# Kernel tuning notes

Measured on AMD Instinct MI355X. Metric: run time of the kernel, lower is better.

## Reference

```python
import jax, jax.numpy as jnp
import numpy as np

B, H, N, D = 64, 12, 196, 768  # ViT-B/16 @ 224: 196 patch tokens + 1 CLS


def setup_inputs() -> dict:
    key = jax.random.key(0)
    k1, k2, k3 = jax.random.split(key, 3)
    student_tokens = jax.random.normal(k1, (B, N, D), dtype=jnp.float32)
    teacher_tokens = jax.random.normal(k2, (B, N, D), dtype=jnp.float32)
    teacher_attn = jax.random.uniform(k3, (B, H, N + 1, N + 1), dtype=jnp.float32)
    return {
        "student_tokens": student_tokens,
        "teacher_tokens": teacher_tokens,
        "teacher_attn": teacher_attn,
    }


def reference(student_tokens, teacher_tokens, teacher_attn):
    s = student_tokens.astype(jnp.float32)
    t = teacher_tokens.astype(jnp.float32)
    # CLS->patch attention, averaged over heads: [B, N]
    w = teacher_attn[:, :, 0, 1:].mean(axis=1)
    w = w / (w.sum(axis=-1, keepdims=True) + 1e-8)
    s = w[..., None] * s
    t = w[..., None] * t
    # center over token dim
    s_c = s - s.mean(axis=1, keepdims=True)
    t_c = t - t.mean(axis=1, keepdims=True)
    tr_s = jnp.sum(s_c * s_c, axis=(1, 2))  # [B]
    tr_t = jnp.sum(t_c * t_c, axis=(1, 2))  # [B]
    # cross-covariance: [B, D, D]
    cross = jnp.einsum("bnd,bne->bde", s_c, t_c)
    # nuclear norm = sum of singular values
    nuclear = jnp.linalg.svd(cross, compute_uv=False).sum(axis=-1)  # [B]
    loss = jnp.maximum(tr_s + tr_t - 2.0 * nuclear, 0.0).mean()
    return loss
```

## Files before the change

### kernel.cpp

```cpp
#include <hip/hip_runtime.h>
#include <hip/hip_bf16.h>
#include <math.h>

#define NTOK 196
#define NDIM 768
#define NB 64
#define NH 12
#define NA 197
#define MAT (NTOK * NTOK)
#define ATTN_HW (NA * NA)
#define POLAR_ITERS 15

#define PADC 208
#define NTILE 13
#define POLAR_LDS_BYTES (2 * NTOK * PADC * 2)

#define GCH 64
#define GPLANE (208 * GCH)
#define GRAM_LDS_BYTES (2 * GPLANE * 2)

#define POW_LD 197
#define POW_F_WORDS (NTOK * POW_LD)
#define POW_LDS_BYTES ((POW_F_WORDS + 2 * NTOK + 256) * 4)

#define PTLD 208
#define TRI_WORDS 19306
#define CHOL2_PT_WORDS (16 * PTLD)
#define CHOL2_TRI_OFF CHOL2_PT_WORDS
#define CHOL2_ROWOFF_OFF (CHOL2_TRI_OFF + TRI_WORDS)
#define CHOL2_PV_OFF 22832
#define CHOL2_LDS_BYTES ((CHOL2_PV_OFF + 32) * 4)

typedef __attribute__((ext_vector_type(8))) short short8;
typedef __attribute__((ext_vector_type(4))) short short4_t;
typedef __attribute__((ext_vector_type(4))) float f32x4;

__device__ inline short8 s8zero() { short8 z = {0,0,0,0,0,0,0,0}; return z; }

__device__ inline short f2bf(float f) {
  union { float f; unsigned u; } v; v.f = f;
  unsigned u = v.u;
  u += 0x7fffu + ((u >> 16) & 1u);
  return (short)(u >> 16);
}
__device__ inline float bf2f(short s) {
  union { unsigned u; float f; } v;
  v.u = ((unsigned)(unsigned short)s) << 16;
  return v.f;
}

__global__ void k_w(const float* __restrict__ attn, float* __restrict__ wbuf) {
  int b = blockIdx.x;
  int tid = threadIdx.x;
  __shared__ float red[256];
  float w0 = 0.f;
  if (tid < NTOK) {
    size_t base = (size_t)b * NH * ATTN_HW + 1 + tid;
    #pragma unroll
    for (int h = 0; h < NH; ++h) w0 += attn[base + (size_t)h * ATTN_HW];
    w0 *= (1.f / NH);
  }
  red[tid] = (tid < NTOK) ? w0 : 0.f;
  __syncthreads();
  for (int s = 128; s > 0; s >>= 1) { if (tid < s) red[tid] += red[tid + s]; __syncthreads(); }
  float S = red[0];
  if (tid < NTOK) wbuf[b * NTOK + tid] = w0 / (S + 1e-8f);
}

__global__ __launch_bounds__(512, 1) void k_gram_mfma(
    const float* __restrict__ s, const float* __restrict__ t,
    const float* __restrict__ wbuf, float* __restrict__ Gbuf) {
  extern __shared__ short gsm[];
  short* bhp = gsm;
  short* blp = gsm + GPLANE;
  __shared__ float wsh[NTOK];
  int slot = blockIdx.x, b = slot >> 1, src = slot & 1;
  const float* X = (src ? t : s) + (size_t)b * NTOK * NDIM;
  int tid = threadIdx.x;
  int wave = tid >> 6, ln15 = tid & 15, quad = (tid >> 4) & 3;

  if (tid < NTOK) wsh[tid] = wbuf[b * NTOK + tid];
  for (int i = tid; i < 768; i += 512) {
    int p = i / 384, o = i - p * 384;
    ((int*)(gsm + p * GPLANE + 196 * GCH))[o] = 0;
  }
  __syncthreads();

  f32x4 zz = {0.f, 0.f, 0.f, 0.f};
  f32x4 acc[12];
  #pragma unroll
  for (int j = 0; j < 12; ++j) acc[j] = zz;

  for (int c = 0; c < NDIM / GCH; ++c) {
    int kc = c * GCH;
    for (int gi = tid; gi < NTOK * 8; gi += 512) {
      int r = gi >> 3, g = gi & 7;
      const float* sp = X + (size_t)r * NDIM + kc + g * 8;
      float4 f0 = *(const float4*)(sp);
      float4 f1 = *(const float4*)(sp + 4);
      float wv = wsh[r];
      float vs[8] = {f0.x, f0.y, f0.z, f0.w, f1.x, f1.y, f1.z, f1.w};
      short8 hv, lv;
      #pragma unroll
      for (int e = 0; e < 8; ++e) {
        float y = wv * vs[e];
        short hb = f2bf(y);
        hv[e] = hb;
        lv[e] = f2bf(y - bf2f(hb));
      }
      int pg = (g ^ (r & 7)) * 8;
      *(short8*)(bhp + r * GCH + pg) = hv;
      *(short8*)(blp + r * GCH + pg) = lv;
    }
    __syncthreads();
    #pragma unroll
    for (int j = 0; j < 12; ++j) {
      int T = wave + 8 * j;
      if (T < 91) {
        int ti = (int)((sqrtf(8.f * T + 1.f) - 1.f) * 0.5f);
        if ((ti + 1) * (ti + 2) / 2 <= T) ++ti;
        if (ti * (ti + 1) / 2 > T) --ti;
        int tj = T - ti * (ti + 1) / 2;
        int ra = ti * 16 + ln15, rb = tj * 16 + ln15;
        #pragma unroll
        for (int ks = 0; ks < 2; ++ks) {
          int gb0 = ks * 4 + quad;
          int ga = (gb0 ^ (ra & 7)) * 8, gb = (gb0 ^ (rb & 7)) * 8;
          short8 ah = *(const short8*)(bhp + ra * GCH + ga);
          short8 al = *(const short8*)(blp + ra * GCH + ga);
          short8 bhf = *(const short8*)(bhp + rb * GCH + gb);
          short8 blf = *(const short8*)(blp + rb * GCH + gb);
          acc[j] = __builtin_amdgcn_mfma_f32_16x16x32_bf16(ah, bhf, acc[j], 0, 0, 0);
          acc[j] = __builtin_amdgcn_mfma_f32_16x16x32_bf16(ah, blf, acc[j], 0, 0, 0);
          acc[j] = __builtin_amdgcn_mfma_f32_16x16x32_bf16(al, bhf, acc[j], 0, 0, 0);
        }
      }
    }
    __syncthreads();
  }

  float* G = Gbuf + (size_t)slot * MAT;
  #pragma unroll
  for (int j = 0; j < 12; ++j) {
    int T = wave + 8 * j;
    if (T < 91) {
      int ti = (int)((sqrtf(8.f * T + 1.f) - 1.f) * 0.5f);
      if ((ti + 1) * (ti + 2) / 2 <= T) ++ti;
      if (ti * (ti + 1) / 2 > T) --ti;
      int tj = T - ti * (ti + 1) / 2;
      int col = tj * 16 + ln15;
      #pragma unroll
      for (int r = 0; r < 4; ++r) {
        int row = ti * 16 + quad * 4 + r;
        if (row < NTOK && col < NTOK) {
          G[row * NTOK + col] = acc[j][r];
          if (ti != tj) G[col * NTOK + row] = acc[j][r];
        }
      }
    }
  }
}

__global__ void k_center(float* __restrict__ Gbuf, float* __restrict__ trPb) {
  int slot = blockIdx.x;
  float* A = Gbuf + (size_t)slot * MAT;
  __shared__ float r[NTOK];
  __shared__ float red[256];
  __shared__ float gsh, dsh;
  int tid = threadIdx.x;
  float acc = 0.f;
  if (tid < NTOK) {
    for (int m = 0; m < NTOK; ++m) acc += A[m * NTOK + tid];
    r[tid] = acc * (1.f / NTOK);
  }
  red[tid] = (tid < NTOK) ? acc * (1.f / NTOK) : 0.f;
  __syncthreads();
  for (int s = 128; s > 0; s >>= 1) { if (tid < s) red[tid] += red[tid + s]; __syncthreads(); }
  float g = red[0] * (1.f / NTOK);
  float tv = (tid < NTOK) ? (A[tid * NTOK + tid] - 2.f * r[tid] + g) : 0.f;
  __syncthreads();
  red[tid] = tv;
  __syncthreads();
  for (int s = 128; s > 0; s >>= 1) { if (tid < s) red[tid] += red[tid + s]; __syncthreads(); }
  if (tid == 0) {
    float tr = red[0];
    trPb[slot] = tr;
    gsh = g;
    dsh = 1e-4f * fmaxf(tr, 0.f) * (1.f / NTOK);
  }
  __syncthreads();
  float gg = gsh, dd = dsh;
  for (int idx = tid; idx < MAT; idx += 256) {
    int n = idx / NTOK, m = idx - n * NTOK;
    float v = A[idx] - r[n] - r[m] + gg;
    if (n == m) v += dd;
    A[idx] = v;
  }
}

__global__ __launch_bounds__(256, 1) void k_chol_panel(float* __restrict__ Gbuf) {
  extern __shared__ float smf[];
  float* Pt = smf;
  float* tri = smf + CHOL2_TRI_OFF;
  int* rowoff = (int*)(smf + CHOL2_ROWOFF_OFF);
  float* pvb = smf + CHOL2_PV_OFF;
  int slot = blockIdx.x;
  float* A = Gbuf + (size_t)slot * MAT;
  int tid = threadIdx.x;
  if (tid < NTOK) rowoff[tid] = tid * (tid + 1) / 2;
  __syncthreads();
  for (int idx = tid; idx < MAT; idx += 256) {
    int i = idx / NTOK, j = idx - i * NTOK;
    if (j <= i) tri[rowoff[i] + j] = A[idx];
  }
  __syncthreads();

  for (int k0 = 0; k0 < NTOK; k0 += 16) {
    int nb = (NTOK - k0 < 16) ? (NTOK - k0) : 16;
    int t = tid;
    int i = k0 + t;
    bool hasrow = (t < NTOK - k0);
    int ro = hasrow ? rowoff[i] : 0;

    float a[16];
    #pragma unroll
    for (int jj = 0; jj < 16; ++jj) a[jj] = 0.f;
    if (hasrow) {
      #pragma unroll
      for (int jj = 0; jj < 16; ++jj)
        if (jj < nb && k0 + jj <= i) a[jj] = tri[ro + k0 + jj];
    }

    #pragma unroll
    for (int jj = 0; jj < 16; ++jj) {
      bool cv = (jj < nb);
      if (cv && hasrow && t >= jj && t < nb) pvb[((jj & 1) << 4) + t] = a[jj];
      __syncthreads();
      if (cv && hasrow && t >= jj) {
        const float* pv = pvb + ((jj & 1) << 4);
        f32x4 p0 = *(const f32x4*)(pv);
        f32x4 p1 = *(const f32x4*)(pv + 4);
        f32x4 p2 = *(const f32x4*)(pv + 8);
        f32x4 p3 = *(const f32x4*)(pv + 12);
        float pvj = (jj < 4) ? p0[jj & 3] : (jj < 8) ? p1[jj & 3]
                   : (jj < 12) ? p2[jj & 3] : p3[jj & 3];
        float sq = sqrtf(fmaxf(pvj, 1e-20f));
        float pivinv = 1.f / sq;
        float v = a[jj] * pivinv;
        a[jj] = v;
        #pragma unroll
        for (int m = 0; m < 16; ++m) {
          if (m > jj) {
            float pvm = (m < 4) ? p0[m & 3] : (m < 8) ? p1[m & 3]
                       : (m < 12) ? p2[m & 3] : p3[m & 3];
            if (m < nb) a[m] -= v * (pvm * pivinv);
          }
        }
      }
    }

    if (hasrow) {
      #pragma unroll
      for (int jj = 0; jj < 16; ++jj)
        if (jj < nb && k0 + jj <= i) tri[ro + k0 + jj] = a[jj];
      if (t >= nb) {
        #pragma unroll
        for (int jj = 0; jj < 16; ++jj)
          if (jj < nb) Pt[jj * PTLD + i] = a[jj];
      }
    }
    __syncthreads();

    int k1 = k0 + nb;
    int nrem = NTOK - k1;
    if (nrem > 0) {
      int ntile = (nrem + 3) >> 2;
      int Ttot = ntile * (ntile + 1) / 2;
      for (int T = tid; T < Ttot; T += 256) {
        float disc = (2.f * ntile + 1.f) * (2.f * ntile + 1.f) - 8.f * (float)T;
        int tm = (int)((2.f * ntile + 1.f - sqrtf(fmaxf(disc, 0.f))) * 0.5f);
        if (tm > ntile - 1) tm = ntile - 1;
        if (tm < 0) tm = 0;
        #define FCOL(c) ((c) * ntile - (((c) * ((c) - 1)) >> 1))
        while (tm + 1 <= ntile - 1 && FCOL(tm + 1) <= T) ++tm;
        while (tm > 0 && FCOL(tm) > T) --tm;
        int ti = tm + (T - FCOL(tm));
        #undef FCOL
        int i0 = k1 + ti * 4, m0 = k1 + tm * 4;
        f32x4 acc0 = {0.f, 0.f, 0.f, 0.f};
        f32x4 acc1 = acc0, acc2 = acc0, acc3 = acc0;
        #pragma unroll
        for (int jj = 0; jj < 16; ++jj) {
          if (jj < nb) {
            f32x4 li = *(const f32x4*)(Pt + jj * PTLD + i0);
            f32x4 lm = *(const f32x4*)(Pt + jj * PTLD + m0);
            acc0 += lm * li[0];
            acc1 += lm * li[1];
            acc2 += lm * li[2];
            acc3 += lm * li[3];
          }
        }
        #define STORE_ROW(r, av)                                        \
          { int ii = i0 + (r);                                          \
            if (ii < NTOK) {                                            \
              int roi = rowoff[ii];                                     \
              if (m0 + 0 <= ii) tri[roi + m0 + 0] -= (av)[0];           \
              if (m0 + 1 <= ii) tri[roi + m0 + 1] -= (av)[1];           \
              if (m0 + 2 <= ii) tri[roi + m0 + 2] -= (av)[2];           \
              if (m0 + 3 <= ii) tri[roi + m0 + 3] -= (av)[3];           \
            } }
        STORE_ROW(0, acc0)
        STORE_ROW(1, acc1)
        STORE_ROW(2, acc2)
        STORE_ROW(3, acc3)
        #undef STORE_ROW
      }
    }
    __syncthreads();
  }

  for (int idx = tid; idx < MAT; idx += 256) {
    int i = idx / NTOK, j = idx - i * NTOK;
    A[idx] = (j <= i) ? tri[rowoff[i] + j] : 0.f;
  }
}

__global__ void k_chol_global(float* __restrict__ Gbuf) {
  int slot = blockIdx.x;
  float* A = Gbuf + (size_t)slot * MAT;
  __shared__ float col[NTOK];
  __shared__ float piv;
  int tid = threadIdx.x;
  for (int k = 0; k < NTOK; ++k) {
    if (tid == 0) { float p = sqrtf(fmaxf(A[k * NTOK + k], 1e-20f)); A[k * NTOK + k] = p; piv = p; }
    __syncthreads();
    float inv = 1.f / piv;
    for (int i = k + 1 + tid; i < NTOK; i += 256) {
      float v = A[i * NTOK + k] * inv;
      A[i * NTOK + k] = v;
      col[i] = v;
    }
    for (int j = k + 1 + tid; j < NTOK; j += 256) A[k * NTOK + j] = 0.f;
    __syncthreads();
    int nrem = NTOK - 1 - k;
    int total = nrem * (nrem + 1) / 2;
    for (int tt = tid; tt < total; tt += 256) {
      int a = (int)((sqrtf(8.f * tt + 1.f) - 1.f) * 0.5f);
      while ((a + 1) * (a + 2) / 2 <= tt) ++a;
      while (a * (a + 1) / 2 > tt) --a;
      int bb = tt - a * (a + 1) / 2;
      int i = k + 1 + a, j = k + 1 + bb;
      A[i * NTOK + j] -= col[i] * col[j];
    }
    __syncthreads();
  }
}

__global__ void k_F(const float* __restrict__ Gbuf, float* __restrict__ Fbuf) {
  int b = blockIdx.y;
  const float* Lp = Gbuf + (size_t)(2 * b) * MAT;
  const float* Lq = Gbuf + (size_t)(2 * b + 1) * MAT;
  int ti = blockIdx.x / 7, tj = blockIdx.x % 7;
  int ri = ti * 32, cj = tj * 32;
  __shared__ float As[32][33], Bs[32][33];
  int tid = threadIdx.x, ty = tid >> 4, tx = tid & 15;
  float a00 = 0, a01 = 0, a10 = 0, a11 = 0;
  for (int k0 = 0; k0 < NTOK; k0 += 32) {
    for (int l = tid; l < 1024; l += 256) {
      int kk = l >> 5, ii = l & 31;
      int krow = k0 + kk;
      As[kk][ii] = (krow < NTOK && ri + ii < NTOK) ? Lp[(size_t)krow * NTOK + ri + ii] : 0.f;
      Bs[kk][ii] = (krow < NTOK && cj + ii < NTOK) ? Lq[(size_t)krow * NTOK + cj + ii] : 0.f;
    }
    __syncthreads();
    #pragma unroll
    for (int kk = 0; kk < 32; ++kk) {
      float p0 = As[kk][ty], p1 = As[kk][ty + 16];
      float q0 = Bs[kk][tx], q1 = Bs[kk][tx + 16];
      a00 += p0 * q0; a01 += p0 * q1; a10 += p1 * q0; a11 += p1 * q1;
    }
    __syncthreads();
  }
  float* F = Fbuf + (size_t)b * MAT;
  int i0 = ri + ty, i1 = ri + ty + 16, j0 = cj + tx, j1 = cj + tx + 16;
  if (i0 < NTOK && j0 < NTOK) F[i0 * NTOK + j0] = a00;
  if (i0 < NTOK && j1 < NTOK) F[i0 * NTOK + j1] = a01;
  if (i1 < NTOK && j0 < NTOK) F[i1 * NTOK + j0] = a10;
  if (i1 < NTOK && j1 < NTOK) F[i1 * NTOK + j1] = a11;
}

__global__ __launch_bounds__(256, 1) void k_pow_lds(const float* __restrict__ Fbuf,
                                                    float* __restrict__ nrmb) {
  extern __shared__ float psm[];
  float* Fsh = psm;
  float* v = psm + POW_F_WORDS;
  float* u = v + NTOK;
  float* red = u + NTOK;
  int b = blockIdx.x;
  const float* F = Fbuf + (size_t)b * MAT;
  int tid = threadIdx.x;
  for (int idx = tid; idx < MAT; idx += 256) {
    int i = idx / NTOK, j = idx - i * NTOK;
    Fsh[i * POW_LD + j] = F[idx];
  }
  if (tid < NTOK) v[tid] = 1.f;
  __syncthreads();
  float lastsum = 1.f;
  for (int it = 0; it < 6; ++it) {
    if (tid < NTOK) {
      float a = 0.f;
      for (int j = 0; j < NTOK; ++j) a += Fsh[tid * POW_LD + j] * v[j];
      u[tid] = a;
    }
    __syncthreads();
    float a2 = 0.f;
    if (tid < NTOK) { for (int i = 0; i < NTOK; ++i) a2 += Fsh[i * POW_LD + tid] * u[i]; }
    red[tid] = (tid < NTOK) ? a2 * a2 : 0.f;
    __syncthreads();
    for (int s2 = 128; s2 > 0; s2 >>= 1) { if (tid < s2) red[tid] += red[tid + s2]; __syncthreads(); }
    float sum = red[0];
    lastsum = sum;
    float invn = rsqrtf(sum + 1e-30f);
    __syncthreads();
    if (tid < NTOK) v[tid] = a2 * invn;
    __syncthreads();
  }
  if (tid == 0) {
    float sig = sqrtf(sqrtf(lastsum));
    nrmb[b] = 1.f / (1.1f * sig + 1e-30f);
  }
}

__global__ void k_pow(const float* __restrict__ Fbuf, float* __restrict__ nrmb) {
  int b = blockIdx.x;
  const float* F = Fbuf + (size_t)b * MAT;
  __shared__ float v[NTOK], u[NTOK];
  __shared__ float red[256];
  int tid = threadIdx.x;
  if (tid < NTOK) v[tid] = 1.f;
  __syncthreads();
  float lastsum = 1.f;
  for (int it = 0; it < 6; ++it) {
    float a = 0.f;
    if (tid < NTOK) { for (int j = 0; j < NTOK; ++j) a += F[tid * NTOK + j] * v[j]; }
    __syncthreads();
    if (tid < NTOK) u[tid] = a;
    __syncthreads();
    float a2 = 0.f;
    if (tid < NTOK) { for (int i = 0; i < NTOK; ++i) a2 += F[i * NTOK + tid] * u[i]; }
    red[tid] = (tid < NTOK) ? a2 * a2 : 0.f;
    __syncthreads();
    for (int s = 128; s > 0; s >>= 1) { if (tid < s) red[tid] += red[tid + s]; __syncthreads(); }
    float sum = red[0];
    lastsum = sum;
    float invn = rsqrtf(sum + 1e-30f);
    __syncthreads();
    if (tid < NTOK) v[tid] = a2 * invn;
    __syncthreads();
  }
  if (tid == 0) {
    float sig = sqrtf(sqrtf(lastsum));
    nrmb[b] = 1.f / (1.1f * sig + 1e-30f);
  }
}

__global__ void k_scale(const float* __restrict__ Fbuf, const float* __restrict__ nrmb,
                        float* __restrict__ X) {
  int b = blockIdx.y;
  int idx = blockIdx.x * 256 + threadIdx.x;
  if (idx < MAT) X[(size_t)b * MAT + idx] = Fbuf[(size_t)b * MAT + idx] * nrmb[b];
}

__global__ __launch_bounds__(512, 1) void k_polar_fused(
    const float* __restrict__ Fbuf, const float* __restrict__ nrmb,
    float* __restrict__ Xout) {
  extern __shared__ short sm[];
  short* bufA = sm;
  short* bufB = sm + NTOK * PADC;
  int b = blockIdx.x;
  const float* F = Fbuf + (size_t)b * MAT;
  float* XO = Xout + (size_t)b * MAT;
  int tid = threadIdx.x;
  int wave = tid >> 6, ln15 = tid & 15, quad = (tid >> 4) & 3;
  int rt0 = wave, rt1 = wave + 8;
  bool has2 = (rt1 < NTILE);

  for (int q = tid; q < (2 * NTOK * PADC) / 8; q += 512) {
    int4 z = {0, 0, 0, 0};
    ((int4*)sm)[q] = z;
  }
  __syncthreads();
  float invc = nrmb[b];
  for (int q = tid; q < MAT / 4; q += 512) {
    int idx = q * 4;
    int i = idx / NTOK, j = idx - i * NTOK;
    float4 f = ((const float4*)F)[q];
    short4_t w;
    w[0] = f2bf(f.x * invc); w[1] = f2bf(f.y * invc);
    w[2] = f2bf(f.z * invc); w[3] = f2bf(f.w * invc);
    *(short4_t*)(bufA + i * PADC + j) = w;
  }
  __syncthreads();

  int arow0 = rt0 * 16 + ln15;
  int arow1 = rt1 * 16 + ln15;
  bool av1 = has2 && (arow1 < NTOK);
  int m0a = rt0 * 16 + quad * 4;
  int m1a = rt1 * 16 + quad * 4;

  for (int it = 0; it < POLAR_ITERS; ++it) {
    short8 g0[7], g1[7];
    #pragma unroll
    for (int ks = 0; ks < 7; ++ks) {
      int kk = ks * 32 + quad * 8;
      short8 v0 = s8zero(), v1 = s8zero();
      if (kk < PADC) {
        #pragma unroll
        for (int j = 0; j < 8; ++j) {
          v0[j] = bufA[(kk + j) * PADC + arow0];
          if (has2) v1[j] = bufA[(kk + j) * PADC + arow1];
        }
      }
      g0[ks] = v0; g1[ks] = v1;
    }
    {
      short8 a0[7], a1[7];
      #pragma unroll
      for (int ks = 0; ks < 7; ++ks) {
        int kk = ks * 32 + quad * 8;
        a0[ks] = (kk < PADC) ? *(const short8*)(bufA + arow0 * PADC + kk) : s8zero();
        a1[ks] = (av1 && kk < PADC) ? *(const short8*)(bufA + arow1 * PADC + kk) : s8zero();
      }
      for (int ct = 0; ct < NTILE; ++ct) {
        int brow = ct * 16 + ln15;
        bool bv = brow < NTOK;
        f32x4 acc0 = {0.f, 0.f, 0.f, 0.f};
        f32x4 acc1 = {0.f, 0.f, 0.f, 0.f};
        if (ct == rt0) {
          #pragma unroll
          for (int ks = 0; ks < 7; ++ks) {
            acc0 = __builtin_amdgcn_mfma_f32_16x16x32_bf16(a0[ks], a0[ks], acc0, 0, 0, 0);
            if (has2)
              acc1 = __builtin_amdgcn_mfma_f32_16x16x32_bf16(a1[ks], a0[ks], acc1, 0, 0, 0);
          }
        } else if (has2 && ct == rt1) {
          #pragma unroll
          for (int ks = 0; ks < 7; ++ks) {
            acc0 = __builtin_amdgcn_mfma_f32_16x16x32_bf16(a0[ks], a1[ks], acc0, 0, 0, 0);
            acc1 = __builtin_amdgcn_mfma_f32_16x16x32_bf16(a1[ks], a1[ks], acc1, 0, 0, 0);
          }
        } else {
          #pragma unroll
          for (int ks = 0; ks < 7; ++ks) {
            int kk = ks * 32 + quad * 8;
            short8 bfr = (bv && kk < PADC) ? *(const short8*)(bufA + brow * PADC + kk)
                                           : s8zero();
            acc0 = __builtin_amdgcn_mfma_f32_16x16x32_bf16(a0[ks], bfr, acc0, 0, 0, 0);
            if (has2)
              acc1 = __builtin_amdgcn_mfma_f32_16x16x32_bf16(a1[ks], bfr, acc1, 0, 0, 0);
          }
        }
        if (bv) {
          short4_t w0;
          #pragma unroll
          for (int r = 0; r < 4; ++r) {
            float h = -0.5f * acc0[r] + ((m0a + r == brow) ? 1.5f : 0.f);
            w0[r] = f2bf(h);
          }
          *(short4_t*)(bufB + brow * PADC + m0a) = w0;
          if (has2) {
            short4_t w1;
            #pragma unroll
            for (int r = 0; r < 4; ++r) {
              float h = -0.5f * acc1[r] + ((m1a + r == brow) ? 1.5f : 0.f);
              w1[r] = f2bf(h);
            }
            *(short4_t*)(bufB + brow * PADC + m1a) = w1;
          }
        }
      }
    }
    __syncthreads();
    {
      for (int ct = 0; ct < NTILE; ++ct) {
        int n = ct * 16 + ln15;
        bool nv = n < NTOK;
        f32x4 acc0 = {0.f, 0.f, 0.f, 0.f};
        f32x4 acc1 = {0.f, 0.f, 0.f, 0.f};
        #pragma unroll
        for (int ks = 0; ks < 7; ++ks) {
          int kk = ks * 32 + quad * 8;
          short8 bfr = (nv && kk < PADC) ? *(const short8*)(bufB + n * PADC + kk)
                                         : s8zero();
          acc0 = __builtin_amdgcn_mfma_f32_16x16x32_bf16(g0[ks], bfr, acc0, 0, 0, 0);
          if (has2)
            acc1 = __builtin_amdgcn_mfma_f32_16x16x32_bf16(g1[ks], bfr, acc1, 0, 0, 0);
        }
        if (nv) {
          short4_t w0;
          #pragma unroll
          for (int r = 0; r < 4; ++r) w0[r] = f2bf(acc0[r]);
          *(short4_t*)(bufA + n * PADC + m0a) = w0;
          if (has2) {
            short4_t w1;
            #pragma unroll
            for (int r = 0; r < 4; ++r) w1[r] = f2bf(acc1[r]);
            *(short4_t*)(bufA + n * PADC + m1a) = w1;
          }
        }
      }
    }
    __syncthreads();
  }

  for (int q = tid; q < MAT / 4; q += 512) {
    int idx = q * 4;
    int i = idx / NTOK, j = idx - i * NTOK;
    short4_t w = *(const short4_t*)(bufA + i * PADC + j);
    float4 f;
    f.x = bf2f(w[0]); f.y = bf2f(w[1]); f.z = bf2f(w[2]); f.w = bf2f(w[3]);
    ((float4*)XO)[q] = f;
  }
}

__global__ void k_xtx(const float* __restrict__ Xb, float* __restrict__ Gp) {
  int b = blockIdx.y;
  const float* X = Xb + (size_t)b * MAT;
  int x = blockIdx.x, ti = 0;
  while (x >= ti + 1) { x -= ti + 1; ++ti; }
  int tj = x;
  int ri = ti * 32, cj = tj * 32;
  __shared__ float As[32][33], Bs[32][33];
  int tid = threadIdx.x, ty = tid >> 4, tx = tid & 15;
  float a00 = 0, a01 = 0, a10 = 0, a11 = 0;
  for (int k0 = 0; k0 < NTOK; k0 += 32) {
    for (int l = tid; l < 1024; l += 256) {
      int kk = l >> 5, ii = l & 31;
      int krow = k0 + kk;
      As[kk][ii] = (krow < NTOK && ri + ii < NTOK) ? X[(size_t)krow * NTOK + ri + ii] : 0.f;
      Bs[kk][ii] = (krow < NTOK && cj + ii < NTOK) ? X[(size_t)krow * NTOK + cj + ii] : 0.f;
    }
    __syncthreads();
    #pragma unroll
    for (int kk = 0; kk < 32; ++kk) {
      float p0 = As[kk][ty], p1 = As[kk][ty + 16];
      float q0 = Bs[kk][tx], q1 = Bs[kk][tx + 16];
      a00 += p0 * q0; a01 += p0 * q1; a10 += p1 * q0; a11 += p1 * q1;
    }
    __syncthreads();
  }
  float* G = Gp + (size_t)b * MAT;
  int i0 = ri + ty, i1 = ri + ty + 16, j0 = cj + tx, j1 = cj + tx + 16;
  if (i0 < NTOK && j0 < NTOK) { G[i0 * NTOK + j0] = a00; G[j0 * NTOK + i0] = a00; }
  if (i0 < NTOK && j1 < NTOK) { G[i0 * NTOK + j1] = a01; G[j1 * NTOK + i0] = a01; }
  if (i1 < NTOK && j0 < NTOK) { G[i1 * NTOK + j0] = a10; G[j0 * NTOK + i1] = a10; }
  if (i1 < NTOK && j1 < NTOK) { G[i1 * NTOK + j1] = a11; G[j1 * NTOK + i1] = a11; }
}

__global__ void k_nsup(const float* __restrict__ Xb, const float* __restrict__ Gp,
                       float* __restrict__ Xn) {
  int b = blockIdx.y;
  const float* X = Xb + (size_t)b * MAT;
  const float* G = Gp + (size_t)b * MAT;
  int ti = blockIdx.x / 7, tj = blockIdx.x % 7;
  int ri = ti * 32, cj = tj * 32;
  __shared__ float As[32][33], Bs[32][33];
  int tid = threadIdx.x, ty = tid >> 4, tx = tid & 15;
  float a00 = 0, a01 = 0, a10 = 0, a11 = 0;
  for (int k0 = 0; k0 < NTOK; k0 += 32) {
    for (int l = tid; l < 1024; l += 256) {
      int rr = l >> 5, cc = l & 31;
      As[rr][cc] = (ri + rr < NTOK && k0 + cc < NTOK) ? X[(size_t)(ri + rr) * NTOK + k0 + cc] : 0.f;
      Bs[rr][cc] = (k0 + rr < NTOK && cj + cc < NTOK) ? G[(size_t)(k0 + rr) * NTOK + cj + cc] : 0.f;
    }
    __syncthreads();
    #pragma unroll
    for (int kk = 0; kk < 32; ++kk) {
      float p0 = As[ty][kk], p1 = As[ty + 16][kk];
      float q0 = Bs[kk][tx], q1 = Bs[kk][tx + 16];
      a00 += p0 * q0; a01 += p0 * q1; a10 += p1 * q0; a11 += p1 * q1;
    }
    __syncthreads();
  }
  float* O = Xn + (size_t)b * MAT;
  int i0 = ri + ty, i1 = ri + ty + 16, j0 = cj + tx, j1 = cj + tx + 16;
  if (i0 < NTOK && j0 < NTOK) O[i0 * NTOK + j0] = 1.5f * X[i0 * NTOK + j0] - 0.5f * a00;
  if (i0 < NTOK && j1 < NTOK) O[i0 * NTOK + j1] = 1.5f * X[i0 * NTOK + j1] - 0.5f * a01;
  if (i1 < NTOK && j0 < NTOK) O[i1 * NTOK + j0] = 1.5f * X[i1 * NTOK + j0] - 0.5f * a10;
  if (i1 < NTOK && j1 < NTOK) O[i1 * NTOK + j1] = 1.5f * X[i1 * NTOK + j1] - 0.5f * a11;
}

__global__ void k_nuc(const float* __restrict__ U, const float* __restrict__ Fbuf,
                      float* __restrict__ nucb) {
  int b = blockIdx.x;
  int tid = threadIdx.x;
  const float* Ub = U + (size_t)b * MAT;
  const float* Fb = Fbuf + (size_t)b * MAT;
  float acc = 0.f;
  for (int idx = tid; idx < MAT; idx += 256) acc += Ub[idx] * Fb[idx];
  __shared__ float red[256];
  red[tid] = acc;
  __syncthreads();
  for (int s = 128; s > 0; s >>= 1) { if (tid < s) red[tid] += red[tid + s]; __syncthreads(); }
  if (tid == 0) nucb[b] = red[0];
}

__global__ void k_final(const float* __restrict__ trPb, const float* __restrict__ nucb,
                        float* __restrict__ out) {
  int tid = threadIdx.x;
  float v = fmaxf(trPb[2 * tid] + trPb[2 * tid + 1] - 2.f * nucb[tid], 0.f);
  #pragma unroll
  for (int off = 32; off; off >>= 1) v += __shfl_down(v, off);
  if (tid == 0) out[0] = v * (1.f / 64.f);
}

extern "C" void kernel_launch(void* const* d_in, const int* in_sizes, int n_in,
                              void* d_out, int out_size, void* d_ws, size_t ws_size,
                              hipStream_t stream) {
  (void)in_sizes; (void)n_in; (void)out_size; (void)ws_size;
  const float* s = (const float*)d_in[0];
  const float* t = (const float*)d_in[1];
  const float* attn = (const float*)d_in[2];
  float* out = (float*)d_out;

  float* W = (float*)d_ws;
  float* Gbuf = W;
  float* Fbuf = Gbuf + (size_t)128 * MAT;
  float* Xbuf = Fbuf + (size_t)64 * MAT;
  float* Xnew = Xbuf + (size_t)64 * MAT;
  float* Gpol = Xnew + (size_t)64 * MAT;
  float* wbuf = Gpol + (size_t)64 * MAT;
  float* trPb = wbuf + (size_t)NB * NTOK;
  float* nucb = trPb + 128;
  float* nrmb = nucb + 64;

  k_w<<<NB, 256, 0, stream>>>(attn, wbuf);
  k_gram_mfma<<<128, 512, GRAM_LDS_BYTES, stream>>>(s, t, wbuf, Gbuf);
  k_center<<<128, 256, 0, stream>>>(Gbuf, trPb);

  hipError_t chol_ok = hipFuncSetAttribute(
      reinterpret_cast<const void*>(k_chol_panel),
      hipFuncAttributeMaxDynamicSharedMemorySize, CHOL2_LDS_BYTES);
  if (chol_ok == hipSuccess) {
    k_chol_panel<<<128, 256, CHOL2_LDS_BYTES, stream>>>(Gbuf);
  } else {
    k_chol_global<<<128, 256, 0, stream>>>(Gbuf);
  }

  k_F<<<dim3(49, 64), 256, 0, stream>>>(Gbuf, Fbuf);

  hipError_t pow_ok = hipFuncSetAttribute(
      reinterpret_cast<const void*>(k_pow_lds),
      hipFuncAttributeMaxDynamicSharedMemorySize, POW_LDS_BYTES);
  if (pow_ok == hipSuccess) {
    k_pow_lds<<<64, 256, POW_LDS_BYTES, stream>>>(Fbuf, nrmb);
  } else {
    k_pow<<<64, 256, 0, stream>>>(Fbuf, nrmb);
  }

  hipError_t fused_ok = hipFuncSetAttribute(
      reinterpret_cast<const void*>(k_polar_fused),
      hipFuncAttributeMaxDynamicSharedMemorySize, POLAR_LDS_BYTES);

  const float* finalX;
  if (fused_ok == hipSuccess) {
    k_polar_fused<<<NB, 512, POLAR_LDS_BYTES, stream>>>(Fbuf, nrmb, Xbuf);
    k_xtx<<<dim3(28, 64), 256, 0, stream>>>(Xbuf, Gpol);
    k_nsup<<<dim3(49, 64), 256, 0, stream>>>(Xbuf, Gpol, Xnew);
    k_xtx<<<dim3(28, 64), 256, 0, stream>>>(Xnew, Gpol);
    k_nsup<<<dim3(49, 64), 256, 0, stream>>>(Xnew, Gpol, Xbuf);
    finalX = Xbuf;
  } else {
    k_scale<<<dim3(151, 64), 256, 0, stream>>>(Fbuf, nrmb, Xbuf);
    float* Xc = Xbuf;
    float* Xn = Xnew;
    for (int it = 0; it < POLAR_ITERS; ++it) {
      k_xtx<<<dim3(28, 64), 256, 0, stream>>>(Xc, Gpol);
      k_nsup<<<dim3(49, 64), 256, 0, stream>>>(Xc, Gpol, Xn);
      float* tmp = Xc; Xc = Xn; Xn = tmp;
    }
    finalX = Xc;
  }

  k_nuc<<<64, 256, 0, stream>>>(finalX, Fbuf, nucb);
  k_final<<<1, 64, 0, stream>>>(trPb, nucb, out);
}
```

Before: 1.065 ms.

## Compute F = Lp^T Lq with split-bf16 MFMA and transposed Cholesky output

Adds an MFMA kernel for the F product that splits fp32 Cholesky factors into high and low bf16 parts and keeps three cross products, to approximate fp32 accuracy while using matrix cores. The Cholesky kernel can now write its factor transposed so the new kernel reads contiguous rows. The launch uses 2 blocks per batch, which leaves most of the GPU idle. The polar kernel is also reworked: diagonal-tile register reuse is removed, the transposed gather moves after the first barrier with an added sync, and the vectorized float4 and short4 loads and stores become scalar, which may cost bandwidth.

```diff
diff --git a/kernel.cpp b/kernel.cpp
--- a/kernel.cpp
+++ b/kernel.cpp
@@ -18,6 +18,13 @@
 #define GCH 64
 #define GPLANE (208 * GCH)
 #define GRAM_LDS_BYTES (2 * GPLANE * 2)
+
+#define FCH 64
+#define FA_ROWS 208
+#define FB_ROWS 112
+#define FAPLANE (FA_ROWS * FCH)
+#define FBPLANE (FB_ROWS * FCH)
+#define FMF_LDS_BYTES ((2 * FAPLANE + 2 * FBPLANE) * 2)
 
 #define POW_LD 197
 #define POW_F_WORDS (NTOK * POW_LD)
@@ -198,7 +205,8 @@
   }
 }
 
-__global__ __launch_bounds__(256, 1) void k_chol_panel(float* __restrict__ Gbuf) {
+__global__ __launch_bounds__(256, 1) void k_chol_panel(float* __restrict__ Gbuf,
+                                                       int transposeOut) {
   extern __shared__ float smf[];
   float* Pt = smf;
   float* tri = smf + CHOL2_TRI_OFF;
@@ -319,9 +327,16 @@
     __syncthreads();
   }
 
-  for (int idx = tid; idx < MAT; idx += 256) {
-    int i = idx / NTOK, j = idx - i * NTOK;
-    A[idx] = (j <= i) ? tri[rowoff[i] + j] : 0.f;
+  if (transposeOut) {
+    for (int idx = tid; idx < MAT; idx += 256) {
+      int r2 = idx / NTOK, c2 = idx - r2 * NTOK;
+      A[idx] = (r2 <= c2) ? tri[rowoff[c2] + r2] : 0.f;
+    }
+  } else {
+    for (int idx = tid; idx < MAT; idx += 256) {
+      int i = idx / NTOK, j = idx - i * NTOK;
+      A[idx] = (j <= i) ? tri[rowoff[i] + j] : 0.f;
+    }
   }
 }
 
@@ -353,6 +368,113 @@
       A[i * NTOK + j] -= col[i] * col[j];
     }
     __syncthreads();
+  }
+}
+
+__global__ __launch_bounds__(512, 1) void k_F_mfma(const float* __restrict__ Gbuf,
+                                                   float* __restrict__ Fbuf) {
+  extern __shared__ short fsm[];
+  short* Ah = fsm;
+  short* Al = Ah + FAPLANE;
+  short* Bh = Al + FAPLANE;
+  short* Bl = Bh + FBPLANE;
+  int half = blockIdx.x, b = blockIdx.y;
+  const float* LTp = Gbuf + (size_t)(2 * b) * MAT;
+  const float* LTq = Gbuf + (size_t)(2 * b + 1) * MAT;
+  int co = half * 112;
+  int tid = threadIdx.x;
+  int wave = tid >> 6, ln15 = tid & 15, quad = (tid >> 4) & 3;
+
+  f32x4 zz = {0.f, 0.f, 0.f, 0.f};
+  f32x4 acc[12];
+  #pragma unroll
+  for (int j = 0; j < 12; ++j) acc[j] = zz;
+
+  for (int c = 0; c < 4; ++c) {
+    int kc = c * FCH;
+    bool fullchunk = (kc + FCH <= NTOK);
+    for (int gi = tid; gi < (FA_ROWS + FB_ROWS) * 8; gi += 512) {
+      bool isA = gi < FA_ROWS * 8;
+      int li = isA ? gi : gi - FA_ROWS * 8;
+      int r = li >> 3, g = li & 7;
+      int grow = isA ? r : co + r;
+      short8 hv = s8zero(), lv = s8zero();
+      if (grow < NTOK) {
+        const float* src = (isA ? LTp : LTq) + (size_t)grow * NTOK + kc + g * 8;
+        if (fullchunk) {
+          float4 f0 = *(const float4*)(src);
+          float4 f1 = *(const float4*)(src + 4);
+          float vs[8] = {f0.x, f0.y, f0.z, f0.w, f1.x, f1.y, f1.z, f1.w};
+          #pragma unroll
+          for (int e = 0; e < 8; ++e) {
+            short hb = f2bf(vs[e]);
+            hv[e] = hb;
+            lv[e] = f2bf(vs[e] - bf2f(hb));
+          }
+        } else {
+          #pragma unroll
+          for (int e = 0; e < 8; ++e) {
+            int k = kc + g * 8 + e;
+            if (k < NTOK) {
+              float y = src[e];
+              short hb = f2bf(y);
+              hv[e] = hb;
+              lv[e] = f2bf(y - bf2f(hb));
+            }
+          }
+        }
+      }
+      int pg = (g ^ (r & 7)) * 8;
+      if (isA) {
+        *(short8*)(Ah + r * FCH + pg) = hv;
+        *(short8*)(Al + r * FCH + pg) = lv;
+      } else {
+        *(short8*)(Bh + r * FCH + pg) = hv;
+        *(short8*)(Bl + r * FCH + pg) = lv;
+      }
+    }
+    __syncthreads();
+    #pragma unroll
+    for (int j = 0; j < 12; ++j) {
+      int T = wave + 8 * j;
+      if (T < 91) {
+        int ti = T / 7, tj = T - ti * 7;
+        if (co + tj * 16 < NTOK) {
+          int ra = ti * 16 + ln15;
+          int rb = tj * 16 + ln15;
+          #pragma unroll
+          for (int ks = 0; ks < 2; ++ks) {
+            int gb0 = ks * 4 + quad;
+            int ga = (gb0 ^ (ra & 7)) * 8, gb = (gb0 ^ (rb & 7)) * 8;
+            short8 ah = *(const short8*)(Ah + ra * FCH + ga);
+            short8 al = *(const short8*)(Al + ra * FCH + ga);
+            short8 bh = *(const short8*)(Bh + rb * FCH + gb);
+            short8 bl = *(const short8*)(Bl + rb * FCH + gb);
+            acc[j] = __builtin_amdgcn_mfma_f32_16x16x32_bf16(ah, bh, acc[j], 0, 0, 0);
+            acc[j] = __builtin_amdgcn_mfma_f32_16x16x32_bf16(ah, bl, acc[j], 0, 0, 0);
+            acc[j] = __builtin_amdgcn_mfma_f32_16x16x32_bf16(al, bh, acc[j], 0, 0, 0);
+          }
+        }
+      }
+    }
+    __syncthreads();
+  }
+
+  float* F = Fbuf + (size_t)b * MAT;
+  #pragma unroll
+  for (int j = 0; j < 12; ++j) {
+    int T = wave + 8 * j;
+    if (T < 91) {
+      int ti = T / 7, tj = T - ti * 7;
+      int col = co + tj * 16 + ln15;
+      if (col < NTOK) {
+        #pragma unroll
+        for (int r = 0; r < 4; ++r) {
+          int row = ti * 16 + quad * 4 + r;
+          if (row < NTOK) F[row * NTOK + col] = acc[j][r];
+        }
+      }
+    }
   }
 }
 
@@ -485,20 +607,12 @@
   int rt0 = wave, rt1 = wave + 8;
   bool has2 = (rt1 < NTILE);
 
-  for (int q = tid; q < (2 * NTOK * PADC) / 8; q += 512) {
-    int4 z = {0, 0, 0, 0};
-    ((int4*)sm)[q] = z;
-  }
+  for (int i = tid; i < (2 * NTOK * PADC) / 2; i += 512) ((int*)sm)[i] = 0;
   __syncthreads();
   float invc = nrmb[b];
-  for (int q = tid; q < MAT / 4; q += 512) {
-    int idx = q * 4;
+  for (int idx = tid; idx < MAT; idx += 512) {
     int i = idx / NTOK, j = idx - i * NTOK;
-    float4 f = ((const float4*)F)[q];
-    short4_t w;
-    w[0] = f2bf(f.x * invc); w[1] = f2bf(f.y * invc);
-    w[2] = f2bf(f.z * invc); w[3] = f2bf(f.w * invc);
-    *(short4_t*)(bufA + i * PADC + j) = w;
+    bufA[i * PADC + j] = f2bf(F[idx] * invc);
   }
   __syncthreads();
 
@@ -509,20 +623,6 @@
   int m1a = rt1 * 16 + quad * 4;
 
   for (int it = 0; it < POLAR_ITERS; ++it) {
-    short8 g0[7], g1[7];
-    #pragma unroll
-    for (int ks = 0; ks < 7; ++ks) {
-      int kk = ks * 32 + quad * 8;
-      short8 v0 = s8zero(), v1 = s8zero();
-      if (kk < PADC) {
-        #pragma unroll
-        for (int j = 0; j < 8; ++j) {
-          v0[j] = bufA[(kk + j) * PADC + arow0];
-          if (has2) v1[j] = bufA[(kk + j) * PADC + arow1];
-        }
-      }
-      g0[ks] = v0; g1[ks] = v1;
-    }
     {
       short8 a0[7], a1[7];
       #pragma unroll
@@ -536,29 +636,13 @@
         bool bv = brow < NTOK;
         f32x4 acc0 = {0.f, 0.f, 0.f, 0.f};
         f32x4 acc1 = {0.f, 0.f, 0.f, 0.f};
-        if (ct == rt0) {
-          #pragma unroll
-          for (int ks = 0; ks < 7; ++ks) {
-            acc0 = __builtin_amdgcn_mfma_f32_16x16x32_bf16(a0[ks], a0[ks], acc0, 0, 0, 0);
-            if (has2)
-              acc1 = __builtin_amdgcn_mfma_f32_16x16x32_bf16(a1[ks], a0[ks], acc1, 0, 0, 0);
-          }
-        } else if (has2 && ct == rt1) {
-          #pragma unroll
-          for (int ks = 0; ks < 7; ++ks) {
-            acc0 = __builtin_amdgcn_mfma_f32_16x16x32_bf16(a0[ks], a1[ks], acc0, 0, 0, 0);
-            acc1 = __builtin_amdgcn_mfma_f32_16x16x32_bf16(a1[ks], a1[ks], acc1, 0, 0, 0);
-          }
-        } else {
-          #pragma unroll
-          for (int ks = 0; ks < 7; ++ks) {
-            int kk = ks * 32 + quad * 8;
-            short8 bfr = (bv && kk < PADC) ? *(const short8*)(bufA + brow * PADC + kk)
-                                           : s8zero();
-            acc0 = __builtin_amdgcn_mfma_f32_16x16x32_bf16(a0[ks], bfr, acc0, 0, 0, 0);
-            if (has2)
-              acc1 = __builtin_amdgcn_mfma_f32_16x16x32_bf16(a1[ks], bfr, acc1, 0, 0, 0);
-          }
+        #pragma unroll
+        for (int ks = 0; ks < 7; ++ks) {
+          int kk = ks * 32 + quad * 8;
+          short8 bfr = (bv && kk < PADC) ? *(const short8*)(bufA + brow * PADC + kk) : s8zero();
+          acc0 = __builtin_amdgcn_mfma_f32_16x16x32_bf16(a0[ks], bfr, acc0, 0, 0, 0);
+          if (has2)
+            acc1 = __builtin_amdgcn_mfma_f32_16x16x32_bf16(a1[ks], bfr, acc1, 0, 0, 0);
         }
         if (bv) {
           short4_t w0;
@@ -582,6 +666,21 @@
     }
     __syncthreads();
     {
+      short8 g0[7], g1[7];
+      #pragma unroll
+      for (int ks = 0; ks < 7; ++ks) {
+        int kk = ks * 32 + quad * 8;
+        short8 v0 = s8zero(), v1 = s8zero();
+        if (kk < PADC) {
+          #pragma unroll
+          for (int j = 0; j < 8; ++j) {
+            v0[j] = bufA[(kk + j) * PADC + arow0];
+            if (has2) v1[j] = bufA[(kk + j) * PADC + arow1];
+          }
+        }
+        g0[ks] = v0; g1[ks] = v1;
+      }
+      __syncthreads();
       for (int ct = 0; ct < NTILE; ++ct) {
         int n = ct * 16 + ln15;
         bool nv = n < NTOK;
@@ -590,8 +689,7 @@
         #pragma unroll
         for (int ks = 0; ks < 7; ++ks) {
           int kk = ks * 32 + quad * 8;
-          short8 bfr = (nv && kk < PADC) ? *(const short8*)(bufB + n * PADC + kk)
-                                         : s8zero();
+          short8 bfr = (nv && kk < PADC) ? *(const short8*)(bufB + n * PADC + kk) : s8zero();
           acc0 = __builtin_amdgcn_mfma_f32_16x16x32_bf16(g0[ks], bfr, acc0, 0, 0, 0);
           if (has2)
             acc1 = __builtin_amdgcn_mfma_f32_16x16x32_bf16(g1[ks], bfr, acc1, 0, 0, 0);
@@ -613,13 +711,9 @@
     __syncthreads();
   }
 
-  for (int q = tid; q < MAT / 4; q += 512) {
-    int idx = q * 4;
+  for (int idx = tid; idx < MAT; idx += 512) {
     int i = idx / NTOK, j = idx - i * NTOK;
-    short4_t w = *(const short4_t*)(bufA + i * PADC + j);
-    float4 f;
-    f.x = bf2f(w[0]); f.y = bf2f(w[1]); f.z = bf2f(w[2]); f.w = bf2f(w[3]);
-    ((float4*)XO)[q] = f;
+    XO[idx] = bf2f(bufA[i * PADC + j]);
   }
 }
 
@@ -741,13 +835,22 @@
   hipError_t chol_ok = hipFuncSetAttribute(
       reinterpret_cast<const void*>(k_chol_panel),
       hipFuncAttributeMaxDynamicSharedMemorySize, CHOL2_LDS_BYTES);
+  hipError_t fmf_ok = hipFuncSetAttribute(
+      reinterpret_cast<const void*>(k_F_mfma),
+      hipFuncAttributeMaxDynamicSharedMemorySize, FMF_LDS_BYTES);
+  bool mfmaF = (chol_ok == hipSuccess) && (fmf_ok == hipSuccess);
+
   if (chol_ok == hipSuccess) {
-    k_chol_panel<<<128, 256, CHOL2_LDS_BYTES, stream>>>(Gbuf);
+    k_chol_panel<<<128, 256, CHOL2_LDS_BYTES, stream>>>(Gbuf, mfmaF ? 1 : 0);
   } else {
     k_chol_global<<<128, 256, 0, stream>>>(Gbuf);
   }
 
-  k_F<<<dim3(49, 64), 256, 0, stream>>>(Gbuf, Fbuf);
+  if (mfmaF) {
+    k_F_mfma<<<dim3(2, 64), 512, FMF_LDS_BYTES, stream>>>(Gbuf, Fbuf);
+  } else {
+    k_F<<<dim3(49, 64), 256, 0, stream>>>(Gbuf, Fbuf);
+  }
 
   hipError_t pow_ok = hipFuncSetAttribute(
       reinterpret_cast<const void*>(k_pow_lds),
```

After: 944.4 us. 11.3% less time.
